# Kernel tuning notes

Measured on AMD Instinct MI355X. Metric: run time of the kernel, lower is better.

Reference implementation:

```python
import jax, jax.numpy as jnp
import numpy as np

# Classifier3Stage core of Reg_3stage (giga_depth), defaults: close_far_separation=False, c3_line_div=1
BS, CIN, H, W = 1, 128, 112, 320
CL = (16, 16, 16)          # classes per stage
PAD = (0, 8, 8)
C12 = CL[0] * CL[1]        # 256
C123 = C12 * CL[2]         # 4096
C1D = [128, 32, 32, CL[0] + 2 * PAD[0]]   # per-line grouped conv dims: 128->32->32->16
C2D = [128, 32, 32, CL[1] + 2 * PAD[1]]   # CondMul stage2 dims: 128->32->32->32
C3D = [128, 32, 32, CL[2] + 2 * PAD[2]]   # CondMul stage3 dims (in=ch_latent[0][i], out=ch_latent[1][i+1])


def setup_inputs() -> dict:
    key = jax.random.key(0)

    def p(i, shape):
        return jax.random.normal(jax.random.fold_in(key, i), shape, jnp.float32) * 0.05

    d = {"x_in": jax.random.normal(jax.random.fold_in(key, 0), (BS, CIN, H, W), jnp.float32)}
    for i in range(3):  # c1: per-line (grouped) 1x1 convs -> [H, out, in] weights
        d[f"w1_{i}"] = p(10 + 2 * i, (H, C1D[i + 1], C1D[i]))
        d[f"b1_{i}"] = p(11 + 2 * i, (H, C1D[i + 1]))
    for i in range(3):  # c2: CondMul over H*classes0 conditions
        d[f"w2_{i}"] = p(20 + 2 * i, (H * CL[0], C2D[i], C2D[i + 1]))
        d[f"b2_{i}"] = p(21 + 2 * i, (H * CL[0], C2D[i + 1]))
    for i in range(3):  # c3: CondMul over H*classes12 conditions
        d[f"w3_{i}"] = p(30 + 2 * i, (H * C12, C3D[i], C3D[i + 1]))
        d[f"b3_{i}"] = p(31 + 2 * i, (H * C12, C3D[i + 1]))
    return d


def _lrelu(v):
    return jnp.where(v >= 0, v, 0.01 * v)


def _condmul(x, inds, w, b):
    # x: [N, Cin], inds: [N] int32, w: [K, Cin, Cout], b: [K, Cout]
    return jnp.einsum('ni,nio->no', x, w[inds]) + b[inds]


def reference(x_in, w1_0, b1_0, w1_1, b1_1, w1_2, b1_2,
              w2_0, b2_0, w2_1, b2_1, w2_2, b2_2,
              w3_0, b3_0, w3_1, b3_1, w3_2, b3_2):
    bs, C, h, w = x_in.shape
    x = jnp.transpose(x_in, (0, 2, 3, 1))              # [bs,H,W,C] (far segment = x_in, per-line layout)
    # stage 1: per-line 1x1 grouped convs
    t = x
    for (wt, bt, last) in [(w1_0, b1_0, False), (w1_1, b1_1, False), (w1_2, b1_2, True)]:
        t = jnp.einsum('bhwi,hoi->bhwo', t, wt) + bt[None, :, None, :]
        if not last:
            t = _lrelu(t)
    inds1 = jnp.argmax(t, axis=-1).astype(jnp.int32)   # [bs,H,W]
    off = jnp.arange(h, dtype=jnp.int32)[None, :, None]
    x_l = x.reshape(-1, C)                             # rows in (b,h,w) order
    i1l = (inds1 + CL[0] * off).reshape(-1)
    # stage 2: CondMul chain routed by line*class1 index
    y = _lrelu(_condmul(x_l, i1l, w2_0, b2_0))
    y = _lrelu(_condmul(y, i1l, w2_1, b2_1))
    y = _condmul(y, i1l, w2_2, b2_2)                   # [N, 32]
    inds2 = jnp.argmax(y, axis=1).astype(jnp.int32).reshape(bs, h, w)
    inds12 = inds1 * CL[1] + (inds2 - PAD[1])
    i12l = (jnp.clip(inds12, 0, C12 - 1) + C12 * off).reshape(-1)  # c3_line_div=1 -> scaled == unscaled
    # stage 3: CondMul chain routed by line*classes12 index (close segment = x_in)
    z = _lrelu(_condmul(x_l, i12l, w3_0, b3_0))
    z = _lrelu(_condmul(z, i12l, w3_1, b3_1))
    z = _condmul(z, i12l, w3_2, b3_2)                  # [N, 32]
    inds3 = jnp.argmax(z, axis=1).astype(jnp.int32).reshape(bs, h, w)
    inds123 = jnp.clip(inds12 * CL[2] + (inds3 - PAD[2]), 0, C123 - 1)
    return inds123.reshape(bs, 1, h, w)
```

## Files before the change

kernel.cpp:

```cpp
#include <hip/hip_runtime.h>

#define HH   112
#define WW   320
#define CIN_ 128
#define HW_  (HH * WW)
#define CHUNK 32

__device__ __forceinline__ float lrelu(float v) {
    return v >= 0.f ? v : 0.01f * v;
}

__global__ __launch_bounds__(512, 2)
void k1_stage1(const float* __restrict__ x_in,
               const float* __restrict__ w1_0, const float* __restrict__ b1_0,
               const float* __restrict__ w1_1, const float* __restrict__ b1_1,
               const float* __restrict__ w1_2, const float* __restrict__ b1_2,
               int* __restrict__ inds1_out, float* __restrict__ xT_out,
               int* __restrict__ qc2, int* __restrict__ qc3)
{
    __shared__ float w1s0[32][CIN_ + 1];
    __shared__ float w1s1[32][33];
    __shared__ float w1s2[16][33];
    __shared__ float b1s[80];
    __shared__ float xT[32][132];
    __shared__ float ys[8][4][32];

    const int h   = blockIdx.x >> 1;
    const int q   = blockIdx.x & 1;
    const int tid = threadIdx.x;
    const int base = h * WW;

    if (blockIdx.x == 0 && tid == 0) { *qc2 = 0; *qc3 = 0; }

    for (int n = tid; n < 32 * CIN_; n += 512)
        w1s0[n >> 7][n & 127] = w1_0[h * (32 * CIN_) + n];
    for (int n = tid; n < 32 * 32; n += 512)
        w1s1[n >> 5][n & 31] = w1_1[h * 1024 + n];
    if (tid < 16 * 32)
        w1s2[tid >> 5][tid & 31] = w1_2[h * 512 + tid];
    if      (tid < 32) b1s[tid] = b1_0[h * 32 + tid];
    else if (tid < 64) b1s[tid] = b1_1[h * 32 + (tid - 32)];
    else if (tid < 80) b1s[tid] = b1_2[h * 16 + (tid - 64)];
    __syncthreads();

    const int wave = tid >> 6;
    const int lane = tid & 63;
    const int o    = lane & 31;
    const int half = lane >> 5;
    const int o16  = lane & 15;

    for (int t = 0; t < 5; ++t) {
        const int w0 = q * 160 + t * 32;
        for (int n = tid; n < 32 * CIN_; n += 512) {
            int ww = n & 31, c = n >> 5;
            xT[ww][c] = x_in[c * HW_ + base + w0 + ww];
        }
        __syncthreads();
        for (int n = tid; n < 32 * CIN_; n += 512) {
            int pix = n >> 7, c = n & 127;
            xT_out[(size_t)(base + w0 + pix) * CIN_ + c] = xT[pix][c];
        }

        float a0 = 0.f, a1 = 0.f, a2 = 0.f, a3 = 0.f;
        #pragma unroll
        for (int i = 0; i < 64; i += 4) {
            const int ii = half * 64 + i;
            const float w0v = w1s0[o][ii];
            const float w1v = w1s0[o][ii + 1];
            const float w2v = w1s0[o][ii + 2];
            const float w3v = w1s0[o][ii + 3];
            const float4 v0 = *reinterpret_cast<const float4*>(&xT[wave * 4 + 0][ii]);
            const float4 v1 = *reinterpret_cast<const float4*>(&xT[wave * 4 + 1][ii]);
            const float4 v2 = *reinterpret_cast<const float4*>(&xT[wave * 4 + 2][ii]);
            const float4 v3 = *reinterpret_cast<const float4*>(&xT[wave * 4 + 3][ii]);
            a0 += v0.x * w0v; a1 += v1.x * w0v; a2 += v2.x * w0v; a3 += v3.x * w0v;
            a0 += v0.y * w1v; a1 += v1.y * w1v; a2 += v2.y * w1v; a3 += v3.y * w1v;
            a0 += v0.z * w2v; a1 += v1.z * w2v; a2 += v2.z * w2v; a3 += v3.z * w2v;
            a0 += v0.w * w3v; a1 += v1.w * w3v; a2 += v2.w * w3v; a3 += v3.w * w3v;
        }
        a0 += __shfl_xor(a0, 32); a1 += __shfl_xor(a1, 32);
        a2 += __shfl_xor(a2, 32); a3 += __shfl_xor(a3, 32);
        ys[wave][0][o] = lrelu(a0 + b1s[o]);
        ys[wave][1][o] = lrelu(a1 + b1s[o]);
        ys[wave][2][o] = lrelu(a2 + b1s[o]);
        ys[wave][3][o] = lrelu(a3 + b1s[o]);

        a0 = a1 = a2 = a3 = 0.f;
        #pragma unroll
        for (int i = 0; i < 32; i += 4) {
            const float w0v = w1s1[o][i];
            const float w1v = w1s1[o][i + 1];
            const float w2v = w1s1[o][i + 2];
            const float w3v = w1s1[o][i + 3];
            const float4 y0 = *reinterpret_cast<const float4*>(&ys[wave][0][i]);
            const float4 y1 = *reinterpret_cast<const float4*>(&ys[wave][1][i]);
            const float4 y2 = *reinterpret_cast<const float4*>(&ys[wave][2][i]);
            const float4 y3 = *reinterpret_cast<const float4*>(&ys[wave][3][i]);
            a0 += y0.x * w0v; a1 += y1.x * w0v; a2 += y2.x * w0v; a3 += y3.x * w0v;
            a0 += y0.y * w1v; a1 += y1.y * w1v; a2 += y2.y * w1v; a3 += y3.y * w1v;
            a0 += y0.z * w2v; a1 += y1.z * w2v; a2 += y2.z * w2v; a3 += y3.z * w2v;
            a0 += y0.w * w3v; a1 += y1.w * w3v; a2 += y2.w * w3v; a3 += y3.w * w3v;
        }
        ys[wave][0][o] = lrelu(a0 + b1s[32 + o]);
        ys[wave][1][o] = lrelu(a1 + b1s[32 + o]);
        ys[wave][2][o] = lrelu(a2 + b1s[32 + o]);
        ys[wave][3][o] = lrelu(a3 + b1s[32 + o]);

        a0 = a1 = a2 = a3 = 0.f;
        #pragma unroll
        for (int i = 0; i < 32; i += 4) {
            const float w0v = w1s2[o16][i];
            const float w1v = w1s2[o16][i + 1];
            const float w2v = w1s2[o16][i + 2];
            const float w3v = w1s2[o16][i + 3];
            const float4 y0 = *reinterpret_cast<const float4*>(&ys[wave][0][i]);
            const float4 y1 = *reinterpret_cast<const float4*>(&ys[wave][1][i]);
            const float4 y2 = *reinterpret_cast<const float4*>(&ys[wave][2][i]);
            const float4 y3 = *reinterpret_cast<const float4*>(&ys[wave][3][i]);
            a0 += y0.x * w0v; a1 += y1.x * w0v; a2 += y2.x * w0v; a3 += y3.x * w0v;
            a0 += y0.y * w1v; a1 += y1.y * w1v; a2 += y2.y * w1v; a3 += y3.y * w1v;
            a0 += y0.z * w2v; a1 += y1.z * w2v; a2 += y2.z * w2v; a3 += y3.z * w2v;
            a0 += y0.w * w3v; a1 += y1.w * w3v; a2 += y2.w * w3v; a3 += y3.w * w3v;
        }
        float bv0 = a0 + b1s[64 + o16], bv1 = a1 + b1s[64 + o16];
        float bv2 = a2 + b1s[64 + o16], bv3 = a3 + b1s[64 + o16];
        int bi0 = o16, bi1 = o16, bi2 = o16, bi3 = o16;
        #pragma unroll
        for (int d = 1; d < 16; d <<= 1) {
            const float ov0 = __shfl_xor(bv0, d); const int oi0 = __shfl_xor(bi0, d);
            const float ov1 = __shfl_xor(bv1, d); const int oi1 = __shfl_xor(bi1, d);
            const float ov2 = __shfl_xor(bv2, d); const int oi2 = __shfl_xor(bi2, d);
            const float ov3 = __shfl_xor(bv3, d); const int oi3 = __shfl_xor(bi3, d);
            if (ov0 > bv0 || (ov0 == bv0 && oi0 < bi0)) { bv0 = ov0; bi0 = oi0; }
            if (ov1 > bv1 || (ov1 == bv1 && oi1 < bi1)) { bv1 = ov1; bi1 = oi1; }
            if (ov2 > bv2 || (ov2 == bv2 && oi2 < bi2)) { bv2 = ov2; bi2 = oi2; }
            if (ov3 > bv3 || (ov3 == bv3 && oi3 < bi3)) { bv3 = ov3; bi3 = oi3; }
        }
        if (lane == 0) {
            inds1_out[base + w0 + wave * 4 + 0] = bi0;
            inds1_out[base + w0 + wave * 4 + 1] = bi1;
            inds1_out[base + w0 + wave * 4 + 2] = bi2;
            inds1_out[base + w0 + wave * 4 + 3] = bi3;
        }
        __syncthreads();
    }
}

template <int BINS>
__global__ void sorter(const int* __restrict__ inds_in, int clipmax,
                       int* __restrict__ sorted, int4* __restrict__ queue,
                       int* __restrict__ qcount)
{
    __shared__ int cnt[BINS];
    __shared__ int scan[BINS];
    __shared__ int rank[BINS];

    const int h = blockIdx.x, tid = threadIdx.x, base = h * WW;
    if (tid < BINS) { cnt[tid] = 0; rank[tid] = 0; }
    __syncthreads();

    int c = -1;
    if (tid < WW) {
        c = inds_in[base + tid];
        c = min(max(c, 0), clipmax);
        atomicAdd(&cnt[c], 1);
    }
    __syncthreads();
    if (tid < BINS) scan[tid] = cnt[tid];
    __syncthreads();
    for (int s = 1; s < BINS; s <<= 1) {
        int v = 0;
        if (tid >= s && tid < BINS) v = scan[tid - s];
        __syncthreads();
        if (tid < BINS) scan[tid] += v;
        __syncthreads();
    }
    if (tid < WW) {
        int pos = (scan[c] - cnt[c]) + atomicAdd(&rank[c], 1);
        sorted[base + pos] = base + tid;
    }
    if (tid < BINS && cnt[tid] > 0) {
        int offc = scan[tid] - cnt[tid];
        for (int s0 = 0; s0 < cnt[tid]; s0 += CHUNK) {
            int qi = atomicAdd(qcount, 1);
            queue[qi] = make_int4(h, tid, base + offc + s0,
                                  min(CHUNK, cnt[tid] - s0));
        }
    }
}

#define QK_ROUND(TB, PA, PB, PC, PD)                                           \
{                                                                              \
    float a0 = 0.f, a1 = 0.f, a2 = 0.f, a3 = 0.f;                              \
    _Pragma("unroll")                                                          \
    for (int i = 0; i < 64; i += 4) {                                          \
        const int ii = half * 64 + i;                                          \
        const float w0v = ws0[(ii + 0) * 32 + o];                              \
        const float w1v = ws0[(ii + 1) * 32 + o];                              \
        const float w2v = ws0[(ii + 2) * 32 + o];                              \
        const float w3v = ws0[(ii + 3) * 32 + o];                              \
        const float4 v0 = *reinterpret_cast<const float4*>(&xbuf[wave*4+0][ii]);\
        const float4 v1 = *reinterpret_cast<const float4*>(&xbuf[wave*4+1][ii]);\
        const float4 v2 = *reinterpret_cast<const float4*>(&xbuf[wave*4+2][ii]);\
        const float4 v3 = *reinterpret_cast<const float4*>(&xbuf[wave*4+3][ii]);\
        a0 += v0.x * w0v; a1 += v1.x * w0v; a2 += v2.x * w0v; a3 += v3.x * w0v;\
        a0 += v0.y * w1v; a1 += v1.y * w1v; a2 += v2.y * w1v; a3 += v3.y * w1v;\
        a0 += v0.z * w2v; a1 += v1.z * w2v; a2 += v2.z * w2v; a3 += v3.z * w2v;\
        a0 += v0.w * w3v; a1 += v1.w * w3v; a2 += v2.w * w3v; a3 += v3.w * w3v;\
    }                                                                          \
    a0 += __shfl_xor(a0, 32); a1 += __shfl_xor(a1, 32);                        \
    a2 += __shfl_xor(a2, 32); a3 += __shfl_xor(a3, 32);                        \
    ys[wave][0][o] = lrelu(a0 + bs[o]);                                        \
    ys[wave][1][o] = lrelu(a1 + bs[o]);                                        \
    ys[wave][2][o] = lrelu(a2 + bs[o]);                                        \
    ys[wave][3][o] = lrelu(a3 + bs[o]);                                        \
    a0 = a1 = a2 = a3 = 0.f;                                                   \
    _Pragma("unroll")                                                          \
    for (int i = 0; i < 32; i += 4) {                                          \
        const float w0v = ws1[(i + 0) * 32 + o];                               \
        const float w1v = ws1[(i + 1) * 32 + o];                               \
        const float w2v = ws1[(i + 2) * 32 + o];                               \
        const float w3v = ws1[(i + 3) * 32 + o];                               \
        const float4 y0 = *reinterpret_cast<const float4*>(&ys[wave][0][i]);   \
        const float4 y1 = *reinterpret_cast<const float4*>(&ys[wave][1][i]);   \
        const float4 y2 = *reinterpret_cast<const float4*>(&ys[wave][2][i]);   \
        const float4 y3 = *reinterpret_cast<const float4*>(&ys[wave][3][i]);   \
        a0 += y0.x * w0v; a1 += y1.x * w0v; a2 += y2.x * w0v; a3 += y3.x * w0v;\
        a0 += y0.y * w1v; a1 += y1.y * w1v; a2 += y2.y * w1v; a3 += y3.y * w1v;\
        a0 += y0.z * w2v; a1 += y1.z * w2v; a2 += y2.z * w2v; a3 += y3.z * w2v;\
        a0 += y0.w * w3v; a1 += y1.w * w3v; a2 += y2.w * w3v; a3 += y3.w * w3v;\
    }                                                                          \
    ys[wave][0][o] = lrelu(a0 + bs[32 + o]);                                   \
    ys[wave][1][o] = lrelu(a1 + bs[32 + o]);                                   \
    ys[wave][2][o] = lrelu(a2 + bs[32 + o]);                                   \
    ys[wave][3][o] = lrelu(a3 + bs[32 + o]);                                   \
    a0 = a1 = a2 = a3 = 0.f;                                                   \
    _Pragma("unroll")                                                          \
    for (int i = 0; i < 32; i += 4) {                                          \
        const float w0v = ws2[(i + 0) * 32 + o];                               \
        const float w1v = ws2[(i + 1) * 32 + o];                               \
        const float w2v = ws2[(i + 2) * 32 + o];                               \
        const float w3v = ws2[(i + 3) * 32 + o];                               \
        const float4 y0 = *reinterpret_cast<const float4*>(&ys[wave][0][i]);   \
        const float4 y1 = *reinterpret_cast<const float4*>(&ys[wave][1][i]);   \
        const float4 y2 = *reinterpret_cast<const float4*>(&ys[wave][2][i]);   \
        const float4 y3 = *reinterpret_cast<const float4*>(&ys[wave][3][i]);   \
        a0 += y0.x * w0v; a1 += y1.x * w0v; a2 += y2.x * w0v; a3 += y3.x * w0v;\
        a0 += y0.y * w1v; a1 += y1.y * w1v; a2 += y2.y * w1v; a3 += y3.y * w1v;\
        a0 += y0.z * w2v; a1 += y1.z * w2v; a2 += y2.z * w2v; a3 += y3.z * w2v;\
        a0 += y0.w * w3v; a1 += y1.w * w3v; a2 += y2.w * w3v; a3 += y3.w * w3v;\
    }                                                                          \
    float bv0 = a0 + bs[64 + o], bv1 = a1 + bs[64 + o];                        \
    float bv2 = a2 + bs[64 + o], bv3 = a3 + bs[64 + o];                        \
    int bi0 = o, bi1 = o, bi2 = o, bi3 = o;                                    \
    _Pragma("unroll")                                                          \
    for (int d = 1; d < 32; d <<= 1) {                                         \
        const float ov0 = __shfl_xor(bv0, d); const int oi0 = __shfl_xor(bi0, d);\
        const float ov1 = __shfl_xor(bv1, d); const int oi1 = __shfl_xor(bi1, d);\
        const float ov2 = __shfl_xor(bv2, d); const int oi2 = __shfl_xor(bi2, d);\
        const float ov3 = __shfl_xor(bv3, d); const int oi3 = __shfl_xor(bi3, d);\
        if (ov0 > bv0 || (ov0 == bv0 && oi0 < bi0)) { bv0 = ov0; bi0 = oi0; }  \
        if (ov1 > bv1 || (ov1 == bv1 && oi1 < bi1)) { bv1 = ov1; bi1 = oi1; }  \
        if (ov2 > bv2 || (ov2 == bv2 && oi2 < bi2)) { bv2 = ov2; bi2 = oi2; }  \
        if (ov3 > bv3 || (ov3 == bv3 && oi3 < bi3)) { bv3 = ov3; bi3 = oi3; }  \
    }                                                                          \
    if (lane == 0) {                                                           \
        const int tb4 = (TB) + wave * 4;                                       \
        if (STAGE == 2) {                                                      \
            if (tb4 + 0 < n) result[PA] = c * 16 + bi0 - 8;                    \
            if (tb4 + 1 < n) result[PB] = c * 16 + bi1 - 8;                    \
            if (tb4 + 2 < n) result[PC] = c * 16 + bi2 - 8;                    \
            if (tb4 + 3 < n) result[PD] = c * 16 + bi3 - 8;                    \
        } else {                                                               \
            if (tb4 + 0 < n) result[PA] = min(max(inds12_in[PA] * 16 + bi0 - 8, 0), 4095); \
            if (tb4 + 1 < n) result[PB] = min(max(inds12_in[PB] * 16 + bi1 - 8, 0), 4095); \
            if (tb4 + 2 < n) result[PC] = min(max(inds12_in[PC] * 16 + bi2 - 8, 0), 4095); \
            if (tb4 + 3 < n) result[PD] = min(max(inds12_in[PD] * 16 + bi3 - 8, 0), 4095); \
        }                                                                      \
    }                                                                          \
}

template <int STAGE>
__global__ __launch_bounds__(256, 4)
void qk_compute(const float* __restrict__ xT_in, const int* __restrict__ sorted,
                const int4* __restrict__ queue, const int* __restrict__ qcount,
                const float* __restrict__ W0, const float* __restrict__ Bb0,
                const float* __restrict__ W1, const float* __restrict__ Bb1,
                const float* __restrict__ W2, const float* __restrict__ Bb2,
                const int* __restrict__ inds12_in, int* __restrict__ result)
{
    __shared__ float ws0[CIN_ * 32];
    __shared__ float ws1[32 * 32];
    __shared__ float ws2[32 * 32];
    __shared__ float bs[96];
    __shared__ float xbuf[16][CIN_];
    __shared__ float ys[4][4][32];

    const int tid  = threadIdx.x;
    const int wave = tid >> 6;
    const int lane = tid & 63;
    const int o    = lane & 31;
    const int half = lane >> 5;

    const int qn = *qcount;
    for (int qi = blockIdx.x; qi < qn; qi += gridDim.x) {
        const int4 it4   = queue[qi];
        const int  c     = it4.y;
        const int  start = it4.z;
        const int  n     = it4.w;
        const int  key   = (STAGE == 2) ? (it4.x * 16 + c) : (it4.x * 256 + c);
        const int  nr    = (n + 15) >> 4;
        const int  t0    = wave * 4;

        __syncthreads();

        const int pA0 = sorted[start + min(t0 + 0, n - 1)];
        const int pB0 = sorted[start + min(t0 + 1, n - 1)];
        const int pC0 = sorted[start + min(t0 + 2, n - 1)];
        const int pD0 = sorted[start + min(t0 + 3, n - 1)];
        const float2 xA0 = *reinterpret_cast<const float2*>(&xT_in[(size_t)pA0 * CIN_ + 2 * lane]);
        const float2 xB0 = *reinterpret_cast<const float2*>(&xT_in[(size_t)pB0 * CIN_ + 2 * lane]);
        const float2 xC0 = *reinterpret_cast<const float2*>(&xT_in[(size_t)pC0 * CIN_ + 2 * lane]);
        const float2 xD0 = *reinterpret_cast<const float2*>(&xT_in[(size_t)pD0 * CIN_ + 2 * lane]);

        for (int i = tid; i < 1024; i += 256)
            ((float4*)ws0)[i] = ((const float4*)(W0 + (size_t)key * 4096))[i];
        ((float4*)ws1)[tid] = ((const float4*)(W1 + (size_t)key * 1024))[tid];
        ((float4*)ws2)[tid] = ((const float4*)(W2 + (size_t)key * 1024))[tid];
        if      (tid < 32) bs[tid] = Bb0[(size_t)key * 32 + tid];
        else if (tid < 64) bs[tid] = Bb1[(size_t)key * 32 + (tid - 32)];
        else if (tid < 96) bs[tid] = Bb2[(size_t)key * 32 + (tid - 64)];
        __syncthreads();

        *reinterpret_cast<float2*>(&xbuf[wave * 4 + 0][2 * lane]) = xA0;
        *reinterpret_cast<float2*>(&xbuf[wave * 4 + 1][2 * lane]) = xB0;
        *reinterpret_cast<float2*>(&xbuf[wave * 4 + 2][2 * lane]) = xC0;
        *reinterpret_cast<float2*>(&xbuf[wave * 4 + 3][2 * lane]) = xD0;

        int pA1 = 0, pB1 = 0, pC1 = 0, pD1 = 0;
        float2 xA1 = {0.f, 0.f}, xB1 = {0.f, 0.f}, xC1 = {0.f, 0.f}, xD1 = {0.f, 0.f};
        if (nr == 2) {
            pA1 = sorted[start + min(16 + t0 + 0, n - 1)];
            pB1 = sorted[start + min(16 + t0 + 1, n - 1)];
            pC1 = sorted[start + min(16 + t0 + 2, n - 1)];
            pD1 = sorted[start + min(16 + t0 + 3, n - 1)];
            xA1 = *reinterpret_cast<const float2*>(&xT_in[(size_t)pA1 * CIN_ + 2 * lane]);
            xB1 = *reinterpret_cast<const float2*>(&xT_in[(size_t)pB1 * CIN_ + 2 * lane]);
            xC1 = *reinterpret_cast<const float2*>(&xT_in[(size_t)pC1 * CIN_ + 2 * lane]);
            xD1 = *reinterpret_cast<const float2*>(&xT_in[(size_t)pD1 * CIN_ + 2 * lane]);
        }

        QK_ROUND(0, pA0, pB0, pC0, pD0)

        if (nr == 2) {
            *reinterpret_cast<float2*>(&xbuf[wave * 4 + 0][2 * lane]) = xA1;
            *reinterpret_cast<float2*>(&xbuf[wave * 4 + 1][2 * lane]) = xB1;
            *reinterpret_cast<float2*>(&xbuf[wave * 4 + 2][2 * lane]) = xC1;
            *reinterpret_cast<float2*>(&xbuf[wave * 4 + 3][2 * lane]) = xD1;
            QK_ROUND(16, pA1, pB1, pC1, pD1)
        }
    }
}

__global__ __launch_bounds__(512, 4)
void reg3_fused(const float* __restrict__ x_in,
                const float* __restrict__ w1_0, const float* __restrict__ b1_0,
                const float* __restrict__ w1_1, const float* __restrict__ b1_1,
                const float* __restrict__ w1_2, const float* __restrict__ b1_2,
                const float* __restrict__ w2_0, const float* __restrict__ b2_0,
                const float* __restrict__ w2_1, const float* __restrict__ b2_1,
                const float* __restrict__ w2_2, const float* __restrict__ b2_2,
                const float* __restrict__ w3_0, const float* __restrict__ b3_0,
                const float* __restrict__ w3_1, const float* __restrict__ b3_1,
                const float* __restrict__ w3_2, const float* __restrict__ b3_2,
                int* __restrict__ out)
{
    __shared__ float xT[8][CIN_ + 1];
    __shared__ float w1s0[32][CIN_ + 1];
    __shared__ float w1s1[32][33];
    __shared__ float w1s2[16][33];
    __shared__ float b1s[80];

    const int h   = blockIdx.x / 40;
    const int w0  = (blockIdx.x % 40) * 8;
    const int tid = threadIdx.x;

    for (int n = tid; n < 8 * CIN_; n += 512) {
        int ww = n & 7, c = n >> 3;
        xT[ww][c] = x_in[c * HW_ + h * WW + w0 + ww];
    }
    for (int n = tid; n < 32 * CIN_; n += 512)
        w1s0[n >> 7][n & 127] = w1_0[h * (32 * CIN_) + n];
    for (int n = tid; n < 32 * 32; n += 512)
        w1s1[n >> 5][n & 31] = w1_1[h * 1024 + n];
    if (tid < 16 * 32)
        w1s2[tid >> 5][tid & 31] = w1_2[h * 512 + tid];
    if      (tid < 32) b1s[tid] = b1_0[h * 32 + tid];
    else if (tid < 64) b1s[tid] = b1_1[h * 32 + (tid - 32)];
    else if (tid < 80) b1s[tid] = b1_2[h * 16 + (tid - 64)];
    __syncthreads();

    const int wave = tid >> 6, lane = tid & 63;
    const int o = lane & 31, half = lane >> 5, o16 = lane & 15;
    const float* xr = &xT[wave][0];

    float acc = 0.f;
    #pragma unroll
    for (int i = 0; i < 64; ++i) { int ii = half * 64 + i; acc += xr[ii] * w1s0[o][ii]; }
    acc += __shfl_xor(acc, 32);
    float y = lrelu(acc + b1s[o]);
    acc = 0.f;
    #pragma unroll
    for (int i = 0; i < 32; ++i) acc += __shfl(y, i) * w1s1[o][i];
    float y2 = lrelu(acc + b1s[32 + o]);
    acc = 0.f;
    #pragma unroll
    for (int i = 0; i < 32; ++i) acc += __shfl(y2, i) * w1s2[o16][i];
    float t1 = acc + b1s[64 + o16];

    float bv = t1; int bi = o16;
    #pragma unroll
    for (int d = 1; d < 16; d <<= 1) {
        float ov = __shfl_xor(bv, d); int oi = __shfl_xor(bi, d);
        if (ov > bv || (ov == bv && oi < bi)) { bv = ov; bi = oi; }
    }
    const int inds1 = bi;
    const int idx1  = inds1 + 16 * h;

    const float* Wp = w2_0 + (size_t)idx1 * (CIN_ * 32);
    acc = 0.f;
    #pragma unroll
    for (int i = 0; i < 64; ++i) { int ii = half * 64 + i; acc += xr[ii] * Wp[ii * 32 + o]; }
    acc += __shfl_xor(acc, 32);
    y = lrelu(acc + b2_0[idx1 * 32 + o]);
    Wp = w2_1 + (size_t)idx1 * 1024;
    acc = 0.f;
    #pragma unroll
    for (int i = 0; i < 32; ++i) acc += __shfl(y, i) * Wp[i * 32 + o];
    y2 = lrelu(acc + b2_1[idx1 * 32 + o]);
    Wp = w2_2 + (size_t)idx1 * 1024;
    acc = 0.f;
    #pragma unroll
    for (int i = 0; i < 32; ++i) acc += __shfl(y2, i) * Wp[i * 32 + o];
    float y3 = acc + b2_2[idx1 * 32 + o];

    bv = y3; bi = o;
    #pragma unroll
    for (int d = 1; d < 32; d <<= 1) {
        float ov = __shfl_xor(bv, d); int oi = __shfl_xor(bi, d);
        if (ov > bv || (ov == bv && oi < bi)) { bv = ov; bi = oi; }
    }
    const int inds2  = bi;
    const int inds12 = inds1 * 16 + inds2 - 8;
    const int clip12 = min(max(inds12, 0), 255);
    const int idx12  = clip12 + 256 * h;

    Wp = w3_0 + (size_t)idx12 * (CIN_ * 32);
    acc = 0.f;
    #pragma unroll
    for (int i = 0; i < 64; ++i) { int ii = half * 64 + i; acc += xr[ii] * Wp[ii * 32 + o]; }
    acc += __shfl_xor(acc, 32);
    y = lrelu(acc + b3_0[idx12 * 32 + o]);
    Wp = w3_1 + (size_t)idx12 * 1024;
    acc = 0.f;
    #pragma unroll
    for (int i = 0; i < 32; ++i) acc += __shfl(y, i) * Wp[i * 32 + o];
    y2 = lrelu(acc + b3_1[idx12 * 32 + o]);
    Wp = w3_2 + (size_t)idx12 * 1024;
    acc = 0.f;
    #pragma unroll
    for (int i = 0; i < 32; ++i) acc += __shfl(y2, i) * Wp[i * 32 + o];
    y3 = acc + b3_2[idx12 * 32 + o];

    bv = y3; bi = o;
    #pragma unroll
    for (int d = 1; d < 32; d <<= 1) {
        float ov = __shfl_xor(bv, d); int oi = __shfl_xor(bi, d);
        if (ov > bv || (ov == bv && oi < bi)) { bv = ov; bi = oi; }
    }
    int inds123 = inds12 * 16 + bi - 8;
    inds123 = min(max(inds123, 0), 4095);
    if (lane == 0) out[h * WW + w0 + wave] = inds123;
}

extern "C" void kernel_launch(void* const* d_in, const int* in_sizes, int n_in,
                              void* d_out, int out_size, void* d_ws, size_t ws_size,
                              hipStream_t stream)
{
    const float* x_in = (const float*)d_in[0];
    const float* w1_0 = (const float*)d_in[1];
    const float* b1_0 = (const float*)d_in[2];
    const float* w1_1 = (const float*)d_in[3];
    const float* b1_1 = (const float*)d_in[4];
    const float* w1_2 = (const float*)d_in[5];
    const float* b1_2 = (const float*)d_in[6];
    const float* w2_0 = (const float*)d_in[7];
    const float* b2_0 = (const float*)d_in[8];
    const float* w2_1 = (const float*)d_in[9];
    const float* b2_1 = (const float*)d_in[10];
    const float* w2_2 = (const float*)d_in[11];
    const float* b2_2 = (const float*)d_in[12];
    const float* w3_0 = (const float*)d_in[13];
    const float* b3_0 = (const float*)d_in[14];
    const float* w3_1 = (const float*)d_in[15];
    const float* b3_1 = (const float*)d_in[16];
    const float* w3_2 = (const float*)d_in[17];
    const float* b3_2 = (const float*)d_in[18];
    int* out = (int*)d_out;

    char* ws = (char*)d_ws;
    int*   inds1_ws  = (int*)(ws + 0);
    int*   inds12_ws = (int*)(ws + 143360);
    int*   sorted2   = (int*)(ws + 286720);
    int*   sorted3   = (int*)(ws + 430080);
    int*   qc2       = (int*)(ws + 573440);
    int*   qc3       = (int*)(ws + 573444);
    int4*  queue2    = (int4*)(ws + 573456);
    int4*  queue3    = (int4*)(ws + 1146896);
    float* xT_ws     = (float*)(ws + 1720336);
    const size_t NEED = 1720336 + (size_t)HW_ * CIN_ * 4;

    if (ws_size >= NEED) {
        k1_stage1<<<HH * 2, 512, 0, stream>>>(
            x_in, w1_0, b1_0, w1_1, b1_1, w1_2, b1_2,
            inds1_ws, xT_ws, qc2, qc3);
        sorter<16><<<HH, 512, 0, stream>>>(inds1_ws, 15, sorted2, queue2, qc2);
        qk_compute<2><<<2048, 256, 0, stream>>>(
            xT_ws, sorted2, queue2, qc2,
            w2_0, b2_0, w2_1, b2_1, w2_2, b2_2, nullptr, inds12_ws);
        sorter<256><<<HH, 512, 0, stream>>>(inds12_ws, 255, sorted3, queue3, qc3);
        qk_compute<3><<<2048, 256, 0, stream>>>(
            xT_ws, sorted3, queue3, qc3,
            w3_0, b3_0, w3_1, b3_1, w3_2, b3_2, inds12_ws, out);
    } else {
        reg3_fused<<<HH * 40, 512, 0, stream>>>(
            x_in, w1_0, b1_0, w1_1, b1_1, w1_2, b1_2,
            w2_0, b2_0, w2_1, b2_1, w2_2, b2_2,
            w3_0, b3_0, w3_1, b3_1, w3_2, b3_2, out);
    }
}
```

Before: 181.0 us.

## Fuse per-line sorters into producer kernels via last-block completion counters

Removes the two standalone sorter kernel launches. The last block to finish each line, found with an atomic done counter and threadfence, now runs the bucket sort and queue build inside the stage-1 and stage-2 kernels. Control counters are zeroed by a memset instead of inside stage 1. This saves launch gaps and a pass over the data, but adds atomics and fences and puts serial sort work on the tail blocks.

```diff
diff --git a/kernel.cpp b/kernel.cpp
--- a/kernel.cpp
+++ b/kernel.cpp
@@ -8,6 +8,47 @@
 
 __device__ __forceinline__ float lrelu(float v) {
     return v >= 0.f ? v : 0.01f * v;
+}
+
+template <int BINS, int NT>
+__device__ void sorter_dev(const int* __restrict__ inds_in,
+                           int* __restrict__ sorted, int4* __restrict__ queue,
+                           int* __restrict__ qcount,
+                           int* cnt, int* scan, int* rank, int h)
+{
+    const int tid = threadIdx.x, base = h * WW;
+    if (tid < BINS) { cnt[tid] = 0; rank[tid] = 0; }
+    __syncthreads();
+    for (int p = tid; p < WW; p += NT) {
+        int c = inds_in[base + p];
+        c = min(max(c, 0), BINS - 1);
+        atomicAdd(&cnt[c], 1);
+    }
+    __syncthreads();
+    if (tid < BINS) scan[tid] = cnt[tid];
+    __syncthreads();
+    for (int s = 1; s < BINS; s <<= 1) {
+        int v = 0;
+        if (tid >= s && tid < BINS) v = scan[tid - s];
+        __syncthreads();
+        if (tid < BINS) scan[tid] += v;
+        __syncthreads();
+    }
+    for (int p = tid; p < WW; p += NT) {
+        int c = inds_in[base + p];
+        c = min(max(c, 0), BINS - 1);
+        int pos = (scan[c] - cnt[c]) + atomicAdd(&rank[c], 1);
+        sorted[base + pos] = base + p;
+    }
+    if (tid < BINS && cnt[tid] > 0) {
+        int offc = scan[tid] - cnt[tid];
+        for (int s0 = 0; s0 < cnt[tid]; s0 += CHUNK) {
+            int qi = atomicAdd(qcount, 1);
+            queue[qi] = make_int4(h, tid, base + offc + s0,
+                                  min(CHUNK, cnt[tid] - s0));
+        }
+    }
+    __syncthreads();
 }
 
 __global__ __launch_bounds__(512, 2)
@@ -16,7 +57,8 @@
                const float* __restrict__ w1_1, const float* __restrict__ b1_1,
                const float* __restrict__ w1_2, const float* __restrict__ b1_2,
                int* __restrict__ inds1_out, float* __restrict__ xT_out,
-               int* __restrict__ qc2, int* __restrict__ qc3)
+               int* __restrict__ sorted2, int4* __restrict__ queue2,
+               int* __restrict__ qc2, int* __restrict__ done1)
 {
     __shared__ float w1s0[32][CIN_ + 1];
     __shared__ float w1s1[32][33];
@@ -24,13 +66,13 @@
     __shared__ float b1s[80];
     __shared__ float xT[32][132];
     __shared__ float ys[8][4][32];
+    __shared__ int kcnt[16], kscan[16], krank[16];
+    __shared__ int kflag;
 
     const int h   = blockIdx.x >> 1;
     const int q   = blockIdx.x & 1;
     const int tid = threadIdx.x;
     const int base = h * WW;
-
-    if (blockIdx.x == 0 && tid == 0) { *qc2 = 0; *qc3 = 0; }
 
     for (int n = tid; n < 32 * CIN_; n += 512)
         w1s0[n >> 7][n & 127] = w1_0[h * (32 * CIN_) + n];
@@ -144,48 +186,17 @@
         }
         __syncthreads();
     }
-}
-
-template <int BINS>
-__global__ void sorter(const int* __restrict__ inds_in, int clipmax,
-                       int* __restrict__ sorted, int4* __restrict__ queue,
-                       int* __restrict__ qcount)
-{
-    __shared__ int cnt[BINS];
-    __shared__ int scan[BINS];
-    __shared__ int rank[BINS];
-
-    const int h = blockIdx.x, tid = threadIdx.x, base = h * WW;
-    if (tid < BINS) { cnt[tid] = 0; rank[tid] = 0; }
-    __syncthreads();
-
-    int c = -1;
-    if (tid < WW) {
-        c = inds_in[base + tid];
-        c = min(max(c, 0), clipmax);
-        atomicAdd(&cnt[c], 1);
-    }
-    __syncthreads();
-    if (tid < BINS) scan[tid] = cnt[tid];
-    __syncthreads();
-    for (int s = 1; s < BINS; s <<= 1) {
-        int v = 0;
-        if (tid >= s && tid < BINS) v = scan[tid - s];
-        __syncthreads();
-        if (tid < BINS) scan[tid] += v;
-        __syncthreads();
-    }
-    if (tid < WW) {
-        int pos = (scan[c] - cnt[c]) + atomicAdd(&rank[c], 1);
-        sorted[base + pos] = base + tid;
-    }
-    if (tid < BINS && cnt[tid] > 0) {
-        int offc = scan[tid] - cnt[tid];
-        for (int s0 = 0; s0 < cnt[tid]; s0 += CHUNK) {
-            int qi = atomicAdd(qcount, 1);
-            queue[qi] = make_int4(h, tid, base + offc + s0,
-                                  min(CHUNK, cnt[tid] - s0));
-        }
+
+    if (tid == 0) {
+        __threadfence();
+        int prev = atomicAdd(&done1[h], 1);
+        kflag = (prev == 1) ? 1 : 0;
+    }
+    __syncthreads();
+    if (kflag) {
+        __threadfence();
+        sorter_dev<16, 512>(inds1_out, sorted2, queue2, qc2,
+                            kcnt, kscan, krank, h);
     }
 }
 
@@ -280,14 +291,16 @@
     }                                                                          \
 }
 
-template <int STAGE>
+template <int STAGE, int DOSORT>
 __global__ __launch_bounds__(256, 4)
 void qk_compute(const float* __restrict__ xT_in, const int* __restrict__ sorted,
                 const int4* __restrict__ queue, const int* __restrict__ qcount,
                 const float* __restrict__ W0, const float* __restrict__ Bb0,
                 const float* __restrict__ W1, const float* __restrict__ Bb1,
                 const float* __restrict__ W2, const float* __restrict__ Bb2,
-                const int* __restrict__ inds12_in, int* __restrict__ result)
+                const int* __restrict__ inds12_in, int* __restrict__ result,
+                int* __restrict__ done_px, int* __restrict__ s_sorted,
+                int4* __restrict__ s_queue, int* __restrict__ s_qc)
 {
     __shared__ float ws0[CIN_ * 32];
     __shared__ float ws1[32 * 32];
@@ -295,6 +308,10 @@
     __shared__ float bs[96];
     __shared__ float xbuf[16][CIN_];
     __shared__ float ys[4][4][32];
+    __shared__ int scnt[DOSORT ? 256 : 1];
+    __shared__ int sscan[DOSORT ? 256 : 1];
+    __shared__ int srank[DOSORT ? 256 : 1];
+    __shared__ int sline;
 
     const int tid  = threadIdx.x;
     const int wave = tid >> 6;
@@ -358,6 +375,21 @@
             *reinterpret_cast<float2*>(&xbuf[wave * 4 + 2][2 * lane]) = xC1;
             *reinterpret_cast<float2*>(&xbuf[wave * 4 + 3][2 * lane]) = xD1;
             QK_ROUND(16, pA1, pB1, pC1, pD1)
+        }
+
+        if (DOSORT) {
+            __syncthreads();
+            if (tid == 0) {
+                __threadfence();
+                int d = atomicAdd(&done_px[it4.x], n) + n;
+                sline = (d == WW) ? it4.x : -1;
+            }
+            __syncthreads();
+            if (sline >= 0) {
+                __threadfence();
+                sorter_dev<256, 256>(result, s_sorted, s_queue, s_qc,
+                                     scnt, sscan, srank, sline);
+            }
         }
     }
 }
@@ -513,25 +545,30 @@
     int*   inds12_ws = (int*)(ws + 143360);
     int*   sorted2   = (int*)(ws + 286720);
     int*   sorted3   = (int*)(ws + 430080);
-    int*   qc2       = (int*)(ws + 573440);
-    int*   qc3       = (int*)(ws + 573444);
-    int4*  queue2    = (int4*)(ws + 573456);
-    int4*  queue3    = (int4*)(ws + 1146896);
-    float* xT_ws     = (float*)(ws + 1720336);
-    const size_t NEED = 1720336 + (size_t)HW_ * CIN_ * 4;
+    int*   ctrl      = (int*)(ws + 573440);
+    int4*  queue2    = (int4*)(ws + 574464);
+    int4*  queue3    = (int4*)(ws + 1147904);
+    float* xT_ws     = (float*)(ws + 1721344);
+    const size_t NEED = 1721344 + (size_t)HW_ * CIN_ * 4;
+
+    int* qc2   = ctrl + 0;
+    int* qc3   = ctrl + 1;
+    int* done1 = ctrl + 2;
+    int* done2 = ctrl + 114;
 
     if (ws_size >= NEED) {
+        hipMemsetAsync(ctrl, 0, 1024, stream);
         k1_stage1<<<HH * 2, 512, 0, stream>>>(
             x_in, w1_0, b1_0, w1_1, b1_1, w1_2, b1_2,
-            inds1_ws, xT_ws, qc2, qc3);
-        sorter<16><<<HH, 512, 0, stream>>>(inds1_ws, 15, sorted2, queue2, qc2);
-        qk_compute<2><<<2048, 256, 0, stream>>>(
+            inds1_ws, xT_ws, sorted2, queue2, qc2, done1);
+        qk_compute<2, 1><<<2048, 256, 0, stream>>>(
             xT_ws, sorted2, queue2, qc2,
-            w2_0, b2_0, w2_1, b2_1, w2_2, b2_2, nullptr, inds12_ws);
-        sorter<256><<<HH, 512, 0, stream>>>(inds12_ws, 255, sorted3, queue3, qc3);
-        qk_compute<3><<<2048, 256, 0, stream>>>(
+            w2_0, b2_0, w2_1, b2_1, w2_2, b2_2, nullptr, inds12_ws,
+            done2, sorted3, queue3, qc3);
+        qk_compute<3, 0><<<2048, 256, 0, stream>>>(
             xT_ws, sorted3, queue3, qc3,
-            w3_0, b3_0, w3_1, b3_1, w3_2, b3_2, inds12_ws, out);
+            w3_0, b3_0, w3_1, b3_1, w3_2, b3_2, inds12_ws, out,
+            nullptr, nullptr, nullptr, nullptr);
     } else {
         reg3_fused<<<HH * 40, 512, 0, stream>>>(
             x_in, w1_0, b1_0, w1_1, b1_1, w1_2, b1_2,
```

Result: slower. 257.5 us (+42.3%).
